# Performance work log

Measured on AMD Instinct MI355X. Metric: run time of the kernel, lower is better.

Reference implementation:

```python
import jax, jax.numpy as jnp
import numpy as np

D = 64   # combine_doc_emb_len
H = 2    # heads
B = 256
S = 1024
SIDE = 56  # uid 32 + os 8 + zip 16

def _prelu(x, a):
    return jnp.where(x >= 0, x, a * x)

def _l2norm(x):
    n = jnp.sqrt(jnp.sum(x * x, axis=-1, keepdims=True))
    return x / jnp.maximum(n, 1e-12)

def _attn_branch(x_trans, y_trans, side, w1, b1, a1, w2, b2):
    b, s = x_trans.shape[0], x_trans.shape[1]
    xh = x_trans.reshape(b, s, H, D).transpose(0, 2, 1, 3)   # [B,H,S,D]
    yh = y_trans.reshape(b, 1, H, D).transpose(0, 2, 1, 3)   # [B,H,1,D]
    yhb = jnp.broadcast_to(yh, (b, H, s, D))
    sideb = jnp.broadcast_to(side[:, None, None, :], (b, H, s, side.shape[-1]))
    feat = jnp.concatenate([xh, xh * yhb, xh - yhb, yhb, sideb], axis=-1)  # [B,H,S,4D+SIDE]
    h1 = _prelu(feat @ w1 + b1, a1)          # [B,H,S,40]
    p = (h1 @ w2 + b2)[..., 0]               # [B,H,S]
    out = jnp.einsum('bhsd,bhs->bhd', xh, p).reshape(b, H * D)
    return p, out

def setup_inputs():
    key = jax.random.key(0)
    k = jax.random.split(key, 20)
    def n(i, shape, sc=1.0):
        return sc * jax.random.normal(k[i], shape, dtype=jnp.float32)
    return {
        'local_x_embs': n(0, (B, S, D)),
        'nonlocal_x_embs': n(1, (B, S, D)),
        'y_embs': n(2, (B, D)),
        'user_id_embs': n(3, (B, 32)),
        'os_embs': n(4, (B, 8)),
        'zip_code_embs': n(5, (B, 16)),
        'w_ty': n(6, (D, H * D), 0.05), 'b_ty': n(7, (H * D,), 0.05), 'a_ty': jnp.float32(0.25),
        'w_lx': n(8, (D, H * D), 0.05), 'b_lx': n(9, (H * D,), 0.05), 'a_lx': jnp.float32(0.25),
        'w_nx': n(10, (D, H * D), 0.05), 'b_nx': n(11, (H * D,), 0.05), 'a_nx': jnp.float32(0.25),
        'lw1': n(12, (4 * D + SIDE, 40), 0.05), 'lb1': n(13, (40,), 0.05), 'la1': jnp.float32(0.25),
        'lw2': n(14, (40, 1), 0.05), 'lb2': n(15, (1,), 0.05),
        'nw1': n(16, (4 * D + SIDE, 40), 0.05), 'nb1': n(17, (40,), 0.05), 'na1': jnp.float32(0.25),
        'nw2': n(18, (40, 1), 0.05), 'nb2': n(19, (1,), 0.05),
    }

def reference(local_x_embs, nonlocal_x_embs, y_embs, user_id_embs, os_embs, zip_code_embs, w_ty, b_ty, a_ty, w_lx, b_lx, a_lx, w_nx, b_nx, a_nx, lw1, lb1, la1, lw2, lb2, nw1, nb1, na1, nw2, nb2):
    side = jnp.concatenate([user_id_embs, os_embs, zip_code_embs], axis=-1)  # [B,56]
    local_x_trans = _l2norm(_prelu(local_x_embs @ w_lx + b_lx, a_lx))        # [B,S,H*D]
    nonlocal_x_trans = _l2norm(_prelu(nonlocal_x_embs @ w_nx + b_nx, a_nx))
    y_trans = _l2norm(_prelu(y_embs @ w_ty + b_ty, a_ty))                    # [B,H*D]
    _, local_embs = _attn_branch(local_x_trans, y_trans, side, lw1, lb1, la1, lw2, lb2)
    _, nonlocal_embs = _attn_branch(nonlocal_x_trans, y_trans, side, nw1, nb1, na1, nw2, nb2)
    return (local_embs, nonlocal_embs)
```

## Files before the change

### kernel.cpp

```cpp
#include <hip/hip_runtime.h>

typedef unsigned short u16;
typedef unsigned int   u32;
typedef __attribute__((ext_vector_type(8))) short bf8_t;
typedef __attribute__((ext_vector_type(4))) float f4_t;

#define NB 256
#define NS 1024

__device__ __forceinline__ u16 f2bf(float f){
    u32 u = __float_as_uint(f);
    return (u16)((u + 0x7fffu + ((u >> 16) & 1u)) >> 16);
}
__device__ __forceinline__ u32 pack_trunc(float lo, float hi){
    return (__float_as_uint(hi) & 0xffff0000u) | (__float_as_uint(lo) >> 16);
}

__global__ __launch_bounds__(256) void prep_kernel(
    const float* __restrict__ y,    const float* __restrict__ wty,
    const float* __restrict__ bty,  const float* __restrict__ aty,
    const float* __restrict__ uid,  const float* __restrict__ ose, const float* __restrict__ zipc,
    const float* __restrict__ wlx,  const float* __restrict__ wnx,
    const float* __restrict__ lw1,  const float* __restrict__ lb1,
    const float* __restrict__ nw1,  const float* __restrict__ nb1,
    u32* __restrict__ wtf, u32* __restrict__ weff, float* __restrict__ cs)
{
    const int tid = threadIdx.x;
    const int bx  = blockIdx.x;

    if (bx >= 512) {
        int u = (bx - 512)*256 + tid;
        int lane = u & 63, fr = u >> 6;
        int br = fr >> 4, t = fr & 15, n = t >> 1, ks = t & 1;
        int q = lane >> 4, lm = lane & 15;
        const float* W = br ? wnx : wlx;
        u32 out[4];
        #pragma unroll
        for (int p = 0; p < 4; ++p) {
            int k = ks*32 + q*8 + p*2;
            float lo = W[k*128 + n*16 + lm];
            float hi = W[(k+1)*128 + n*16 + lm];
            out[p] = (u32)f2bf(lo) | ((u32)f2bf(hi) << 16);
        }
        *(uint4*)&wtf[u*4] = make_uint4(out[0], out[1], out[2], out[3]);
        return;
    }

    __shared__ float yl[64];
    __shared__ float sq[128];
    __shared__ float yv[128];
    __shared__ float cpart[240];

    const int b  = bx >> 1;
    const int br = bx & 1;
    const float* w1 = br ? nw1 : lw1;
    const float* b1 = br ? nb1 : lb1;

    if (tid < 64) yl[tid] = y[b*64 + tid];
    __syncthreads();
    float v = 0.f;
    if (tid < 128) {
        float acc = bty[tid];
        for (int k = 0; k < 64; ++k) acc = fmaf(yl[k], wty[k*128 + tid], acc);
        float a = aty[0];
        v = (acc >= 0.f) ? acc : a * acc;
        sq[tid] = v * v;
    }
    __syncthreads();
    for (int s = 64; s >= 1; s >>= 1) { if (tid < s) sq[tid] += sq[tid+s]; __syncthreads(); }
    if (tid < 128) yv[tid] = v * (1.f / fmaxf(sqrtf(sq[0]), 1e-12f));
    __syncthreads();

    for (int u = tid; u < 768; u += 256) {
        int lane = u & 63, fr = u >> 6;
        int h = fr / 6, t = fr % 6, nj = t >> 1, ks = t & 1;
        int q = lane >> 4, lm = lane & 15, j = nj*16 + lm;
        u32 out[4];
        #pragma unroll
        for (int p = 0; p < 4; ++p) {
            u32 w = 0;
            #pragma unroll
            for (int e = 0; e < 2; ++e) {
                int k = ks*32 + q*8 + p*2 + e;
                float val = 0.f;
                if (j < 40)
                    val = w1[k*40 + j] + w1[(128+k)*40 + j] + yv[h*64 + k] * w1[(64+k)*40 + j];
                w |= ((u32)f2bf(val)) << (16*e);
            }
            out[p] = w;
        }
        *(uint4*)&weff[((size_t)(br*NB + b)*12 + fr)*64*4 + lane*4] =
            make_uint4(out[0], out[1], out[2], out[3]);
    }

    if (tid < 240) {
        int cj = tid / 3, sl = tid % 3;
        int h = cj / 40, j = cj % 40;
        float acc = 0.f;
        for (int t = sl*40; t < sl*40 + 40; ++t) {
            if (t < 64) {
                acc = fmaf(yv[h*64 + t], w1[(192+t)*40 + j] - w1[(128+t)*40 + j], acc);
            } else {
                int u = t - 64;
                float sv, wv;
                if (u < 32)      { sv = uid[b*32 + u];        wv = w1[(256+u)*40 + j]; }
                else if (u < 40) { sv = ose[b*8 + (u-32)];    wv = w1[(288+(u-32))*40 + j]; }
                else             { sv = zipc[b*16 + (u-40)];  wv = w1[(296+(u-40))*40 + j]; }
                acc = fmaf(sv, wv, acc);
            }
        }
        cpart[tid] = acc;
    }
    __syncthreads();
    if (tid < 96) {
        int h = tid / 48, jj = tid % 48;
        float val = 0.f;
        if (jj < 40) {
            int cj = h*40 + jj;
            val = b1[jj] + cpart[cj*3] + cpart[cj*3+1] + cpart[cj*3+2];
        }
        cs[(size_t)(br*NB + b)*96 + tid] = val;
    }
}

__global__ __launch_bounds__(256, 2) void main_kernel(
    const float* __restrict__ xloc, const float* __restrict__ xnon,
    const float* __restrict__ blx,  const float* __restrict__ alx,
    const float* __restrict__ bnx,  const float* __restrict__ anx,
    const float* __restrict__ la1,  const float* __restrict__ lw2, const float* __restrict__ lb2,
    const float* __restrict__ na1,  const float* __restrict__ nw2, const float* __restrict__ nb2,
    const u32* __restrict__ wtf, const u32* __restrict__ weff, const float* __restrict__ cs,
    float* __restrict__ out)
{
    __shared__ u16   tn[4*16*136];
    __shared__ float red[512];

    const int tid  = threadIdx.x;
    const int b    = blockIdx.x;
    const int br   = blockIdx.y;
    const int zc   = blockIdx.z;
    const int w    = tid >> 6;
    const int lane = tid & 63;
    const int q    = lane >> 4;
    const int lm   = lane & 15;

    const float* xg   = br ? xnon : xloc;
    const float* bias = br ? bnx  : blx;
    const float  ax   = br ? anx[0] : alx[0];
    const float  a1v  = br ? na1[0] : la1[0];
    const float  b2v  = br ? nb2[0] : lb2[0];
    const float* w2   = br ? nw2  : lw2;

    const bf8_t* wtfv  = (const bf8_t*)wtf;
    const bf8_t* weffv = (const bf8_t*)weff + (size_t)(br*NB + b)*12*64;
    bf8_t Bfrag[8][2];
    #pragma unroll
    for (int n = 0; n < 8; ++n)
        #pragma unroll
        for (int ks = 0; ks < 2; ++ks)
            Bfrag[n][ks] = wtfv[(br*16 + n*2 + ks)*64 + lane];
    bf8_t Cfrag[2][3][2];
    #pragma unroll
    for (int h = 0; h < 2; ++h)
        #pragma unroll
        for (int nj = 0; nj < 3; ++nj)
            #pragma unroll
            for (int ks = 0; ks < 2; ++ks)
                Cfrag[h][nj][ks] = weffv[(h*6 + nj*2 + ks)*64 + lane];

    float bv[8];
    #pragma unroll
    for (int n = 0; n < 8; ++n) bv[n] = bias[n*16 + lm];
    float w2v[3];
    #pragma unroll
    for (int nj = 0; nj < 3; ++nj) w2v[nj] = (nj*16 + lm < 40) ? w2[nj*16 + lm] : 0.f;
    float Cv[2][3];
    #pragma unroll
    for (int h = 0; h < 2; ++h)
        #pragma unroll
        for (int nj = 0; nj < 3; ++nj)
            Cv[h][nj] = cs[(size_t)(br*NB + b)*96 + h*48 + nj*16 + lm];

    u16* tw = &tn[w*2176];
    const f4_t zero4 = {0.f, 0.f, 0.f, 0.f};
    float outp[8];
    #pragma unroll
    for (int n = 0; n < 8; ++n) outp[n] = 0.f;

    const float* xb = &xg[(size_t)b*NS*64];
    #define ROWPTR(it) (xb + (size_t)((zc*8 + ((it)>>2)*4 + w)*64 + ((it)&3)*16 + lm)*64)

    float4 p0, p1, p2, p3;
    {
        const float* xr = ROWPTR(0);
        p0 = *(const float4*)(xr + q*8);
        p1 = *(const float4*)(xr + q*8 + 4);
        p2 = *(const float4*)(xr + 32 + q*8);
        p3 = *(const float4*)(xr + 32 + q*8 + 4);
    }

    #pragma unroll
    for (int it = 0; it < 8; ++it) {
        float4 c0 = p0, c1 = p1, c2 = p2, c3 = p3;
        if (it < 7) {
            const float* xr = ROWPTR(it + 1);
            p0 = *(const float4*)(xr + q*8);
            p1 = *(const float4*)(xr + q*8 + 4);
            p2 = *(const float4*)(xr + 32 + q*8);
            p3 = *(const float4*)(xr + 32 + q*8 + 4);
        }
        union { u32 u[4]; bf8_t v; } A0, A1;
        A0.u[0] = pack_trunc(c0.x, c0.y); A0.u[1] = pack_trunc(c0.z, c0.w);
        A0.u[2] = pack_trunc(c1.x, c1.y); A0.u[3] = pack_trunc(c1.z, c1.w);
        A1.u[0] = pack_trunc(c2.x, c2.y); A1.u[1] = pack_trunc(c2.z, c2.w);
        A1.u[2] = pack_trunc(c3.x, c3.y); A1.u[3] = pack_trunc(c3.z, c3.w);

        float tv[8][4];
        float ssq[4] = {0.f, 0.f, 0.f, 0.f};
        #pragma unroll
        for (int n = 0; n < 8; ++n) {
            f4_t acc = __builtin_amdgcn_mfma_f32_16x16x32_bf16(A0.v, Bfrag[n][0], zero4, 0, 0, 0);
            acc      = __builtin_amdgcn_mfma_f32_16x16x32_bf16(A1.v, Bfrag[n][1], acc,   0, 0, 0);
            #pragma unroll
            for (int r = 0; r < 4; ++r) {
                float vv = acc[r] + bv[n];
                vv = (vv >= 0.f) ? vv : ax * vv;
                tv[n][r] = vv;
                ssq[r] = fmaf(vv, vv, ssq[r]);
            }
        }
        #pragma unroll
        for (int r = 0; r < 4; ++r) {
            float s = ssq[r];
            s += __shfl_xor(s, 1);
            s += __shfl_xor(s, 2);
            s += __shfl_xor(s, 4);
            s += __shfl_xor(s, 8);
            float rinv = 1.f / fmaxf(sqrtf(s), 1e-12f);
            #pragma unroll
            for (int n = 0; n < 8; ++n) tv[n][r] *= rinv;
        }
        #pragma unroll
        for (int n = 0; n < 8; ++n)
            #pragma unroll
            for (int r = 0; r < 4; ++r)
                tw[(q*4+r)*136 + n*16 + lm] = (u16)(__float_as_uint(tv[n][r]) >> 16);

        float pv[2][4];
        #pragma unroll
        for (int h = 0; h < 2; ++h) {
            bf8_t ac0 = *(const bf8_t*)&tw[lm*136 + h*64 + q*8];
            bf8_t ac1 = *(const bf8_t*)&tw[lm*136 + h*64 + 32 + q*8];
            float pp[4] = {0.f, 0.f, 0.f, 0.f};
            #pragma unroll
            for (int nj = 0; nj < 3; ++nj) {
                f4_t acc = __builtin_amdgcn_mfma_f32_16x16x32_bf16(ac0, Cfrag[h][nj][0], zero4, 0, 0, 0);
                acc      = __builtin_amdgcn_mfma_f32_16x16x32_bf16(ac1, Cfrag[h][nj][1], acc,   0, 0, 0);
                #pragma unroll
                for (int r = 0; r < 4; ++r) {
                    float vv = acc[r] + Cv[h][nj];
                    vv = (vv >= 0.f) ? vv : a1v * vv;
                    pp[r] = fmaf(vv, w2v[nj], pp[r]);
                }
            }
            #pragma unroll
            for (int r = 0; r < 4; ++r) {
                float s = pp[r];
                s += __shfl_xor(s, 1);
                s += __shfl_xor(s, 2);
                s += __shfl_xor(s, 4);
                s += __shfl_xor(s, 8);
                pv[h][r] = s + b2v;
            }
        }

        #pragma unroll
        for (int n = 0; n < 8; ++n)
            #pragma unroll
            for (int r = 0; r < 4; ++r)
                outp[n] = fmaf(tv[n][r], pv[n >> 2][r], outp[n]);
    }
    #undef ROWPTR

    #pragma unroll
    for (int n = 0; n < 8; ++n) {
        float vv = outp[n];
        vv += __shfl_xor(vv, 16);
        vv += __shfl_xor(vv, 32);
        outp[n] = vv;
    }
    if (lane < 16) {
        #pragma unroll
        for (int n = 0; n < 8; ++n) red[w*128 + n*16 + lane] = outp[n];
    }
    __syncthreads();
    if (tid < 128) {
        float s = red[tid] + red[128 + tid] + red[256 + tid] + red[384 + tid];
        atomicAdd(&out[((size_t)br*NB + b)*128 + tid], s);
    }
}

extern "C" void kernel_launch(void* const* d_in, const int* in_sizes, int n_in,
                              void* d_out, int out_size, void* d_ws, size_t ws_size,
                              hipStream_t stream)
{
    const float* xl  = (const float*)d_in[0];
    const float* xn  = (const float*)d_in[1];
    const float* y   = (const float*)d_in[2];
    const float* uid = (const float*)d_in[3];
    const float* ose = (const float*)d_in[4];
    const float* zp  = (const float*)d_in[5];
    const float* wty = (const float*)d_in[6];
    const float* bty = (const float*)d_in[7];
    const float* aty = (const float*)d_in[8];
    const float* wlx = (const float*)d_in[9];
    const float* blx = (const float*)d_in[10];
    const float* alx = (const float*)d_in[11];
    const float* wnx = (const float*)d_in[12];
    const float* bnx = (const float*)d_in[13];
    const float* anx = (const float*)d_in[14];
    const float* lw1 = (const float*)d_in[15];
    const float* lb1 = (const float*)d_in[16];
    const float* la1 = (const float*)d_in[17];
    const float* lw2 = (const float*)d_in[18];
    const float* lb2 = (const float*)d_in[19];
    const float* nw1 = (const float*)d_in[20];
    const float* nb1 = (const float*)d_in[21];
    const float* na1 = (const float*)d_in[22];
    const float* nw2 = (const float*)d_in[23];
    const float* nb2 = (const float*)d_in[24];

    u32*   wtf  = (u32*)d_ws;
    u32*   weff = (u32*)((char*)d_ws + 32768);
    float* cs   = (float*)((char*)d_ws + 32768 + 6291456);

    hipMemsetAsync(d_out, 0, (size_t)out_size * sizeof(float), stream);
    prep_kernel<<<dim3(520), dim3(256), 0, stream>>>(
        y, wty, bty, aty, uid, ose, zp, wlx, wnx, lw1, lb1, nw1, nb1, wtf, weff, cs);
    main_kernel<<<dim3(NB, 2, 2), dim3(256), 0, stream>>>(
        xl, xn, blx, alx, bnx, anx,
        la1, lw2, lb2, na1, nw2, nb2,
        wtf, weff, cs, (float*)d_out);
}
```

Before: 245.7 us.

## Transpose MFMA operands, defer L2 normalization, and drop z-split with atomics

The MFMA operand order is swapped so each lane holds four output features of one row. This turns the row-wise norm and p-reductions into two cross-lane shuffles instead of four. The per-row 1/norm scale is pulled out of the second matmul: raw PReLU outputs go to LDS and rinv is applied in the epilogue. Bias is folded into the MFMA accumulator init, PReLU becomes a single fmin+fma, and bias and side constants are staged in shared memory. The z-dimension split is removed, which drops the memset and atomics, so each block covers the whole sequence at the cost of half as many blocks and a longer per-block loop.

Result: slower. 384.1 us (+56.3%).

```diff
diff --git a/kernel.cpp b/kernel.cpp
--- a/kernel.cpp
+++ b/kernel.cpp
@@ -13,7 +13,7 @@
     return (u16)((u + 0x7fffu + ((u >> 16) & 1u)) >> 16);
 }
 __device__ __forceinline__ u32 pack_trunc(float lo, float hi){
-    return (__float_as_uint(hi) & 0xffff0000u) | (__float_as_uint(lo) >> 16);
+    return __builtin_amdgcn_perm(__float_as_uint(hi), __float_as_uint(lo), 0x07060302u);
 }
 
 __global__ __launch_bounds__(256) void prep_kernel(
@@ -134,11 +134,12 @@
 {
     __shared__ u16   tn[4*16*136];
     __shared__ float red[512];
+    __shared__ float bias_sm[128];
+    __shared__ float cs_sm[96];
 
     const int tid  = threadIdx.x;
     const int b    = blockIdx.x;
     const int br   = blockIdx.y;
-    const int zc   = blockIdx.z;
     const int w    = tid >> 6;
     const int lane = tid & 63;
     const int q    = lane >> 4;
@@ -146,10 +147,13 @@
 
     const float* xg   = br ? xnon : xloc;
     const float* bias = br ? bnx  : blx;
-    const float  ax   = br ? anx[0] : alx[0];
-    const float  a1v  = br ? na1[0] : la1[0];
+    const float  am1  = (br ? anx[0] : alx[0]) - 1.f;
+    const float  a1m1 = (br ? na1[0] : la1[0]) - 1.f;
     const float  b2v  = br ? nb2[0] : lb2[0];
     const float* w2   = br ? nw2  : lw2;
+
+    if (tid < 128) bias_sm[tid] = bias[tid];
+    if (tid < 96)  cs_sm[tid]   = cs[(size_t)(br*NB + b)*96 + tid];
 
     const bf8_t* wtfv  = (const bf8_t*)wtf;
     const bf8_t* weffv = (const bf8_t*)weff + (size_t)(br*NB + b)*12*64;
@@ -168,135 +172,135 @@
             for (int ks = 0; ks < 2; ++ks)
                 Cfrag[h][nj][ks] = weffv[(h*6 + nj*2 + ks)*64 + lane];
 
-    float bv[8];
-    #pragma unroll
-    for (int n = 0; n < 8; ++n) bv[n] = bias[n*16 + lm];
-    float w2v[3];
-    #pragma unroll
-    for (int nj = 0; nj < 3; ++nj) w2v[nj] = (nj*16 + lm < 40) ? w2[nj*16 + lm] : 0.f;
-    float Cv[2][3];
-    #pragma unroll
-    for (int h = 0; h < 2; ++h)
-        #pragma unroll
-        for (int nj = 0; nj < 3; ++nj)
-            Cv[h][nj] = cs[(size_t)(br*NB + b)*96 + h*48 + nj*16 + lm];
+    float w2v[3][4];
+    #pragma unroll
+    for (int nj = 0; nj < 3; ++nj)
+        #pragma unroll
+        for (int r = 0; r < 4; ++r) {
+            int j = nj*16 + q*4 + r;
+            w2v[nj][r] = (j < 40) ? w2[j] : 0.f;
+        }
+
+    __syncthreads();
 
     u16* tw = &tn[w*2176];
     const f4_t zero4 = {0.f, 0.f, 0.f, 0.f};
-    float outp[8];
-    #pragma unroll
-    for (int n = 0; n < 8; ++n) outp[n] = 0.f;
+    float outp[8][4];
+    #pragma unroll
+    for (int c = 0; c < 8; ++c)
+        #pragma unroll
+        for (int r = 0; r < 4; ++r) outp[c][r] = 0.f;
 
     const float* xb = &xg[(size_t)b*NS*64];
-    #define ROWPTR(it) (xb + (size_t)((zc*8 + ((it)>>2)*4 + w)*64 + ((it)&3)*16 + lm)*64)
 
     float4 p0, p1, p2, p3;
     {
-        const float* xr = ROWPTR(0);
+        const float* xr = xb + (size_t)(w*64 + lm)*64;
         p0 = *(const float4*)(xr + q*8);
         p1 = *(const float4*)(xr + q*8 + 4);
         p2 = *(const float4*)(xr + 32 + q*8);
         p3 = *(const float4*)(xr + 32 + q*8 + 4);
     }
 
-    #pragma unroll
-    for (int it = 0; it < 8; ++it) {
-        float4 c0 = p0, c1 = p1, c2 = p2, c3 = p3;
-        if (it < 7) {
-            const float* xr = ROWPTR(it + 1);
-            p0 = *(const float4*)(xr + q*8);
-            p1 = *(const float4*)(xr + q*8 + 4);
-            p2 = *(const float4*)(xr + 32 + q*8);
-            p3 = *(const float4*)(xr + 32 + q*8 + 4);
-        }
-        union { u32 u[4]; bf8_t v; } A0, A1;
-        A0.u[0] = pack_trunc(c0.x, c0.y); A0.u[1] = pack_trunc(c0.z, c0.w);
-        A0.u[2] = pack_trunc(c1.x, c1.y); A0.u[3] = pack_trunc(c1.z, c1.w);
-        A1.u[0] = pack_trunc(c2.x, c2.y); A1.u[1] = pack_trunc(c2.z, c2.w);
-        A1.u[2] = pack_trunc(c3.x, c3.y); A1.u[3] = pack_trunc(c3.z, c3.w);
-
-        float tv[8][4];
-        float ssq[4] = {0.f, 0.f, 0.f, 0.f};
-        #pragma unroll
-        for (int n = 0; n < 8; ++n) {
-            f4_t acc = __builtin_amdgcn_mfma_f32_16x16x32_bf16(A0.v, Bfrag[n][0], zero4, 0, 0, 0);
-            acc      = __builtin_amdgcn_mfma_f32_16x16x32_bf16(A1.v, Bfrag[n][1], acc,   0, 0, 0);
-            #pragma unroll
-            for (int r = 0; r < 4; ++r) {
-                float vv = acc[r] + bv[n];
-                vv = (vv >= 0.f) ? vv : ax * vv;
-                tv[n][r] = vv;
-                ssq[r] = fmaf(vv, vv, ssq[r]);
-            }
-        }
+    for (int ss = 0; ss < 4; ++ss) {
+        #pragma unroll
+        for (int rg = 0; rg < 4; ++rg) {
+            float4 c0 = p0, c1 = p1, c2 = p2, c3 = p3;
+            if (rg < 3 || ss < 3) {
+                const int nss = (rg == 3) ? ss + 1 : ss;
+                const int nrg = (rg + 1) & 3;
+                const float* xr = xb + (size_t)((nss*4 + w)*64 + nrg*16 + lm)*64;
+                p0 = *(const float4*)(xr + q*8);
+                p1 = *(const float4*)(xr + q*8 + 4);
+                p2 = *(const float4*)(xr + 32 + q*8);
+                p3 = *(const float4*)(xr + 32 + q*8 + 4);
+            }
+            union { u32 u[4]; bf8_t v; } A0, A1;
+            A0.u[0] = pack_trunc(c0.x, c0.y); A0.u[1] = pack_trunc(c0.z, c0.w);
+            A0.u[2] = pack_trunc(c1.x, c1.y); A0.u[3] = pack_trunc(c1.z, c1.w);
+            A1.u[0] = pack_trunc(c2.x, c2.y); A1.u[1] = pack_trunc(c2.z, c2.w);
+            A1.u[2] = pack_trunc(c3.x, c3.y); A1.u[3] = pack_trunc(c3.z, c3.w);
+
+            float tv[8][4];
+            float s0 = 0.f, s1 = 0.f, s2 = 0.f, s3 = 0.f;
+            #pragma unroll
+            for (int c = 0; c < 8; ++c) {
+                f4_t bi = *(const f4_t*)&bias_sm[c*16 + q*4];
+                f4_t acc = __builtin_amdgcn_mfma_f32_16x16x32_bf16(Bfrag[c][0], A0.v, bi,  0, 0, 0);
+                acc      = __builtin_amdgcn_mfma_f32_16x16x32_bf16(Bfrag[c][1], A1.v, acc, 0, 0, 0);
+                float v0 = acc[0]; v0 = fmaf(fminf(v0, 0.f), am1, v0); tv[c][0] = v0; s0 = fmaf(v0, v0, s0);
+                float v1 = acc[1]; v1 = fmaf(fminf(v1, 0.f), am1, v1); tv[c][1] = v1; s1 = fmaf(v1, v1, s1);
+                float v2 = acc[2]; v2 = fmaf(fminf(v2, 0.f), am1, v2); tv[c][2] = v2; s2 = fmaf(v2, v2, s2);
+                float v3 = acc[3]; v3 = fmaf(fminf(v3, 0.f), am1, v3); tv[c][3] = v3; s3 = fmaf(v3, v3, s3);
+            }
+            float ssq = (s0 + s1) + (s2 + s3);
+            ssq += __shfl_xor(ssq, 16);
+            ssq += __shfl_xor(ssq, 32);
+            const float rinv = 1.f / fmaxf(sqrtf(ssq), 1e-12f);
+
+            #pragma unroll
+            for (int c = 0; c < 8; ++c) {
+                u32 lo = pack_trunc(tv[c][0], tv[c][1]);
+                u32 hi = pack_trunc(tv[c][2], tv[c][3]);
+                *(uint2*)&tw[lm*136 + c*16 + q*4] = make_uint2(lo, hi);
+            }
+
+            float pw[2];
+            #pragma unroll
+            for (int h = 0; h < 2; ++h) {
+                bf8_t ac0 = *(const bf8_t*)&tw[lm*136 + h*64 + q*8];
+                bf8_t ac1 = *(const bf8_t*)&tw[lm*136 + h*64 + 32 + q*8];
+                float pp[3];
+                #pragma unroll
+                for (int nj = 0; nj < 3; ++nj) {
+                    f4_t cv = *(const f4_t*)&cs_sm[h*48 + nj*16 + q*4];
+                    f4_t acc = __builtin_amdgcn_mfma_f32_16x16x32_bf16(Cfrag[h][nj][0], ac0, zero4, 0, 0, 0);
+                    acc      = __builtin_amdgcn_mfma_f32_16x16x32_bf16(Cfrag[h][nj][1], ac1, acc,   0, 0, 0);
+                    float ppl = 0.f;
+                    #pragma unroll
+                    for (int r = 0; r < 4; ++r) {
+                        float vv = fmaf(acc[r], rinv, cv[r]);
+                        vv = fmaf(fminf(vv, 0.f), a1m1, vv);
+                        ppl = fmaf(vv, w2v[nj][r], ppl);
+                    }
+                    pp[nj] = ppl;
+                }
+                float p = (pp[0] + pp[1]) + pp[2];
+                p += __shfl_xor(p, 16);
+                p += __shfl_xor(p, 32);
+                pw[h] = (p + b2v) * rinv;
+            }
+
+            #pragma unroll
+            for (int c = 0; c < 8; ++c)
+                #pragma unroll
+                for (int r = 0; r < 4; ++r)
+                    outp[c][r] = fmaf(tv[c][r], pw[c >> 2], outp[c][r]);
+        }
+    }
+
+    #pragma unroll
+    for (int c = 0; c < 8; ++c)
         #pragma unroll
         for (int r = 0; r < 4; ++r) {
-            float s = ssq[r];
-            s += __shfl_xor(s, 1);
-            s += __shfl_xor(s, 2);
-            s += __shfl_xor(s, 4);
-            s += __shfl_xor(s, 8);
-            float rinv = 1.f / fmaxf(sqrtf(s), 1e-12f);
-            #pragma unroll
-            for (int n = 0; n < 8; ++n) tv[n][r] *= rinv;
-        }
-        #pragma unroll
-        for (int n = 0; n < 8; ++n)
-            #pragma unroll
-            for (int r = 0; r < 4; ++r)
-                tw[(q*4+r)*136 + n*16 + lm] = (u16)(__float_as_uint(tv[n][r]) >> 16);
-
-        float pv[2][4];
-        #pragma unroll
-        for (int h = 0; h < 2; ++h) {
-            bf8_t ac0 = *(const bf8_t*)&tw[lm*136 + h*64 + q*8];
-            bf8_t ac1 = *(const bf8_t*)&tw[lm*136 + h*64 + 32 + q*8];
-            float pp[4] = {0.f, 0.f, 0.f, 0.f};
-            #pragma unroll
-            for (int nj = 0; nj < 3; ++nj) {
-                f4_t acc = __builtin_amdgcn_mfma_f32_16x16x32_bf16(ac0, Cfrag[h][nj][0], zero4, 0, 0, 0);
-                acc      = __builtin_amdgcn_mfma_f32_16x16x32_bf16(ac1, Cfrag[h][nj][1], acc,   0, 0, 0);
-                #pragma unroll
-                for (int r = 0; r < 4; ++r) {
-                    float vv = acc[r] + Cv[h][nj];
-                    vv = (vv >= 0.f) ? vv : a1v * vv;
-                    pp[r] = fmaf(vv, w2v[nj], pp[r]);
-                }
-            }
-            #pragma unroll
-            for (int r = 0; r < 4; ++r) {
-                float s = pp[r];
-                s += __shfl_xor(s, 1);
-                s += __shfl_xor(s, 2);
-                s += __shfl_xor(s, 4);
-                s += __shfl_xor(s, 8);
-                pv[h][r] = s + b2v;
-            }
-        }
-
-        #pragma unroll
-        for (int n = 0; n < 8; ++n)
-            #pragma unroll
-            for (int r = 0; r < 4; ++r)
-                outp[n] = fmaf(tv[n][r], pv[n >> 2][r], outp[n]);
-    }
-    #undef ROWPTR
-
-    #pragma unroll
-    for (int n = 0; n < 8; ++n) {
-        float vv = outp[n];
-        vv += __shfl_xor(vv, 16);
-        vv += __shfl_xor(vv, 32);
-        outp[n] = vv;
-    }
-    if (lane < 16) {
-        #pragma unroll
-        for (int n = 0; n < 8; ++n) red[w*128 + n*16 + lane] = outp[n];
+            float v = outp[c][r];
+            v += __shfl_xor(v, 1);
+            v += __shfl_xor(v, 2);
+            v += __shfl_xor(v, 4);
+            v += __shfl_xor(v, 8);
+            outp[c][r] = v;
+        }
+    if (lm == 0) {
+        #pragma unroll
+        for (int c = 0; c < 8; ++c) {
+            f4_t v = { outp[c][0], outp[c][1], outp[c][2], outp[c][3] };
+            *(f4_t*)&red[w*128 + c*16 + q*4] = v;
+        }
     }
     __syncthreads();
     if (tid < 128) {
-        float s = red[tid] + red[128 + tid] + red[256 + tid] + red[384 + tid];
-        atomicAdd(&out[((size_t)br*NB + b)*128 + tid], s);
+        out[((size_t)br*NB + b)*128 + tid] =
+            red[tid] + red[128 + tid] + red[256 + tid] + red[384 + tid];
     }
 }
 
@@ -334,10 +338,9 @@
     u32*   weff = (u32*)((char*)d_ws + 32768);
     float* cs   = (float*)((char*)d_ws + 32768 + 6291456);
 
-    hipMemsetAsync(d_out, 0, (size_t)out_size * sizeof(float), stream);
     prep_kernel<<<dim3(520), dim3(256), 0, stream>>>(
         y, wty, bty, aty, uid, ose, zp, wlx, wnx, lw1, lb1, nw1, nb1, wtf, weff, cs);
-    main_kernel<<<dim3(NB, 2, 2), dim3(256), 0, stream>>>(
+    main_kernel<<<dim3(NB, 2), dim3(256), 0, stream>>>(
         xl, xn, blx, alx, bnx, anx,
         la1, lw2, lb2, na1, nw2, nb2,
         wtf, weff, cs, (float*)d_out);
```
